# Optimization experiments

Hardware: AMD Instinct MI355X
Metric: run time of the kernel (lower is better)

## Reference

```python
import jax, jax.numpy as jnp
import numpy as np
import math

B, Hdim, Wdim, C = 8, 64, 64, 512
T, TXT = 77, 512
NH, HD = 8, 64  # num_heads, head_dim
TOP_M = 3
CLAMP_LOGIT = 2.0
CONF_THRESH = 0.35
NEG_INF = -1e30


def _ln(x, g, b, eps=1e-5):
    mu = x.mean(-1, keepdims=True)
    var = ((x - mu) ** 2).mean(-1, keepdims=True)
    return (x - mu) * jax.lax.rsqrt(var + eps) * g + b


def _l2norm(x, eps=1e-6):
    n = jnp.sqrt((x * x).sum(-1, keepdims=True))
    return x / jnp.maximum(n, eps)


def setup_inputs() -> dict:
    key = jax.random.key(0)
    ks = jax.random.split(key, 16)
    s = 0.02
    inp = {
        'visual_features': jax.random.normal(ks[0], (B, Hdim, Wdim, C), jnp.float32),
        'text_features': jax.random.normal(ks[1], (B, T, TXT), jnp.float32),
        'ln1_g': jnp.ones((C,), jnp.float32), 'ln1_b': jnp.zeros((C,), jnp.float32),
        'ln2_g': jnp.ones((C,), jnp.float32), 'ln2_b': jnp.zeros((C,), jnp.float32),
        'Wq': jax.random.normal(ks[2], (C, C), jnp.float32) * s, 'bq': jnp.zeros((C,), jnp.float32),
        'Wk': jax.random.normal(ks[3], (TXT, C), jnp.float32) * s, 'bk': jnp.zeros((C,), jnp.float32),
        'Wv': jax.random.normal(ks[4], (TXT, C), jnp.float32) * s, 'bv': jnp.zeros((C,), jnp.float32),
        'Wo': jax.random.normal(ks[5], (C, C), jnp.float32) * s, 'bo': jnp.zeros((C,), jnp.float32),
        'Wg': jax.random.normal(ks[6], (C, 1), jnp.float32) * s, 'bg': jnp.zeros((1,), jnp.float32),
        'W1': jax.random.normal(ks[7], (C, 4 * C), jnp.float32) * s, 'b1': jnp.zeros((4 * C,), jnp.float32),
        'W2': jax.random.normal(ks[8], (4 * C, C), jnp.float32) * s, 'b2': jnp.zeros((C,), jnp.float32),
        'logit_scale': jnp.asarray(math.log(1.0 / 0.07), jnp.float32),
        'alpha': jnp.asarray(0.1, jnp.float32),
    }
    return inp


def reference(visual_features, text_features, ln1_g, ln1_b, ln2_g, ln2_b,
              Wq, bq, Wk, bk, Wv, bv, Wo, bo, Wg, bg, W1, b1, W2, b2,
              logit_scale, alpha):
    b, h, w, c = visual_features.shape
    n = h * w
    # Pre-LN on visual tokens
    x = _ln(visual_features, ln1_g, ln1_b).reshape(b, n, c)
    q_full = x @ Wq + bq                                   # [B,N,C]
    pad_mask = jnp.abs(text_features).sum(-1) <= 1e-6      # [B,T]
    k_full = text_features @ Wk + bk                       # [B,T,C]
    v_full = text_features @ Wv + bv
    # l2-normalize over full channel dim, then split heads
    q = _l2norm(q_full).reshape(b, n, NH, HD)
    k = _l2norm(k_full).reshape(b, T, NH, HD)
    v = v_full.reshape(b, T, NH, HD)
    scale = jnp.exp(jnp.clip(logit_scale, -CLAMP_LOGIT, CLAMP_LOGIT)) / math.sqrt(float(HD))
    sim = jnp.einsum('bnhd,bthd->bnht', q, k) * scale      # [B,N,H,T]
    sim = jnp.where(pad_mask[:, None, None, :], NEG_INF, sim)
    # top-k sparsification: keep top_m per (b,n,h) row
    topv = jax.lax.top_k(sim, TOP_M)[0][..., -1:]
    sim = jnp.where(sim >= topv, sim, NEG_INF)
    attn = jax.nn.softmax(sim, axis=-1)
    attn = attn / jnp.maximum(attn.sum(-1, keepdims=True), 1e-6)
    all_pad = pad_mask.all(axis=1)                         # [B]
    attn = jnp.where(all_pad[:, None, None, None], 0.0, attn)
    # confidence: max-prob * (1 - normalized entropy), mean over heads
    attn_hn = attn.transpose(0, 2, 1, 3)                   # [B,H,N,T]
    maxp = attn_hn.max(-1, keepdims=True)
    t_eff = jnp.maximum((attn_hn > 0).astype(jnp.float32).sum(-1, keepdims=True), 2.0)
    p = jnp.maximum(attn_hn, 1e-8)
    entropy = jnp.maximum(-(p * jnp.log(p)).sum(-1, keepdims=True) / jnp.log(t_eff), 0.0)
    conf = jnp.clip(maxp * (1.0 - entropy), 0.0, 1.0).mean(axis=1)  # [B,N,1]
    bypass = (conf >= CONF_THRESH).astype(attn.dtype)
    aligned = jnp.einsum('bnht,bthd->bnhd', attn, v).reshape(b, n, c)
    aligned = (aligned @ Wo + bo) * bypass
    gate = jax.nn.sigmoid(x @ Wg + bg)                     # [B,N,1]
    y = x + alpha * gate * aligned
    y = _ln(y, ln2_g, ln2_b)
    y = y + (jax.nn.gelu(y @ W1 + b1, approximate=False) @ W2 + b2)
    return y.reshape(b, h, w, c)
```

## Files before the change

kernel.cpp:

```cpp
#include <hip/hip_runtime.h>
#include <stdint.h>

#define BATCH 8
#define NTOK 4096
#define CDIM 512
#define TTXT 77
#define TPAD 80
#define NHEAD 8
#define HDIM 64
#define HID 2048
#define MROWS 32768
#define NEGINF (-1e30f)

typedef __attribute__((ext_vector_type(8))) short short8;
typedef __attribute__((ext_vector_type(4))) float f32x4;

__device__ __forceinline__ float b2f(unsigned short u) {
    union { unsigned int i; float f; } x; x.i = ((unsigned int)u) << 16; return x.f;
}
__device__ __forceinline__ unsigned short f2b(float f) {
    union { float f; unsigned int i; } x; x.f = f;
    unsigned int i = x.i;
    return (unsigned short)((i + 0x7fffu + ((i >> 16) & 1u)) >> 16);
}

__device__ __forceinline__ void gload16(const void* g, void* l) {
    __builtin_amdgcn_global_load_lds(
        (const __attribute__((address_space(1))) unsigned int*)g,
        (__attribute__((address_space(3))) unsigned int*)l, 16, 0, 0);
}

#define OFF_WQT   ((size_t)0)
#define OFF_WKT   (OFF_WQT + 512*512*2)
#define OFF_WVT   (OFF_WKT + 512*512*2)
#define OFF_WOT   (OFF_WVT + 512*512*2)
#define OFF_W1T   (OFF_WOT + 512*512*2)
#define OFF_W2T   (OFF_W1T + (size_t)2048*512*2)
#define OFF_TEXTB (OFF_W2T + (size_t)512*2048*2)
#define OFF_KFB   (OFF_TEXTB + (size_t)640*512*2)
#define OFF_KNRM  (OFF_KFB + (size_t)640*512*2)
#define OFF_VPAD  (OFF_KNRM + (size_t)640*512*2)
#define OFF_PADM  (OFF_VPAD + (size_t)640*512*2)
#define OFF_ALLP  (OFF_PADM + 2560)
#define OFF_GATE  (OFF_ALLP + 256)
#define OFF_BYP   (OFF_GATE + (size_t)MROWS*4)
#define OFF_XB    (OFF_BYP + (size_t)MROWS*4)
#define OFF_BUFB  (OFF_XB + (size_t)MROWS*CDIM*2)
#define OFF_BUFC  (OFF_BUFB + (size_t)MROWS*CDIM*2)
#define OFF_H     (OFF_BUFC + (size_t)MROWS*CDIM*2)
#define WS_NEED   (OFF_H + (size_t)MROWS*HID*2)
#define OFF_VT    OFF_H

__device__ __forceinline__ float waveReduceAdd(float v) {
#pragma unroll
    for (int m = 1; m < 64; m <<= 1) v += __shfl_xor(v, m);
    return v;
}
__device__ __forceinline__ float waveReduceMin(float v) {
#pragma unroll
    for (int m = 1; m < 64; m <<= 1) v = fminf(v, __shfl_xor(v, m));
    return v;
}
__device__ __forceinline__ float red16Max(float v) {
#pragma unroll
    for (int m = 1; m < 16; m <<= 1) v = fmaxf(v, __shfl_xor(v, m));
    return v;
}
__device__ __forceinline__ float red16Add(float v) {
#pragma unroll
    for (int m = 1; m < 16; m <<= 1) v += __shfl_xor(v, m);
    return v;
}

__global__ __launch_bounds__(256) void transpose_kernel(
    const float* __restrict__ in, unsigned short* __restrict__ out, int R, int C)
{
    __shared__ float tile[32][33];
    const int tx = threadIdx.x & 31, ty = threadIdx.x >> 5;
    const int c0 = blockIdx.x * 32, r0 = blockIdx.y * 32;
#pragma unroll
    for (int i = 0; i < 32; i += 8)
        tile[ty + i][tx] = in[(size_t)(r0 + ty + i) * C + c0 + tx];
    __syncthreads();
#pragma unroll
    for (int i = 0; i < 32; i += 8)
        out[(size_t)(c0 + ty + i) * R + r0 + tx] = f2b(tile[tx][ty + i]);
}

__global__ __launch_bounds__(128) void text_prep_kernel(
    const float* __restrict__ text, unsigned short* __restrict__ textb, float* __restrict__ padm)
{
    __shared__ float sred[2];
    const int r = blockIdx.x;
    const int b = r / TPAD, t = r % TPAD;
    const int tid = threadIdx.x;
    if (t < TTXT) {
        float4 v = *(const float4*)(text + ((size_t)(b * TTXT + t)) * 512 + tid * 4);
        float a = fabsf(v.x) + fabsf(v.y) + fabsf(v.z) + fabsf(v.w);
        a = waveReduceAdd(a);
        if ((tid & 63) == 0) sred[tid >> 6] = a;
        __syncthreads();
        float asum = sred[0] + sred[1];
        ushort4 o; o.x = f2b(v.x); o.y = f2b(v.y); o.z = f2b(v.z); o.w = f2b(v.w);
        *(ushort4*)(textb + (size_t)r * 512 + tid * 4) = o;
        if (tid == 0) padm[r] = (asum <= 1e-6f) ? 1.f : 0.f;
    } else {
        ushort4 z; z.x = 0; z.y = 0; z.z = 0; z.w = 0;
        *(ushort4*)(textb + (size_t)r * 512 + tid * 4) = z;
        if (tid == 0) padm[r] = 1.f;
    }
}

__global__ __launch_bounds__(128) void allpad_kernel(
    const float* __restrict__ padm, float* __restrict__ allp)
{
    __shared__ float sred[2];
    const int b = blockIdx.x, tid = threadIdx.x;
    float f = (tid < TTXT) ? padm[b * TPAD + tid] : 1.f;
    f = waveReduceMin(f);
    if ((tid & 63) == 0) sred[tid >> 6] = f;
    __syncthreads();
    if (tid == 0) allp[b] = fminf(sred[0], sred[1]);
}

__global__ __launch_bounds__(128) void ln1_gate_kernel(
    const float* __restrict__ vin, const float* __restrict__ g1, const float* __restrict__ b1v,
    const float* __restrict__ Wg, const float* __restrict__ bg,
    unsigned short* __restrict__ xb, float* __restrict__ gate)
{
    __shared__ float sred[4];
    const int row = blockIdx.x, tid = threadIdx.x;
    const float4 v = *(const float4*)(vin + (size_t)row * 512 + tid * 4);
    float s = v.x + v.y + v.z + v.w;
    float s2 = v.x * v.x + v.y * v.y + v.z * v.z + v.w * v.w;
    s = waveReduceAdd(s); s2 = waveReduceAdd(s2);
    if ((tid & 63) == 0) { sred[tid >> 6] = s; sred[2 + (tid >> 6)] = s2; }
    __syncthreads();
    s = sred[0] + sred[1]; s2 = sred[2] + sred[3];
    const float mu = s * (1.f / 512.f);
    float var = s2 * (1.f / 512.f) - mu * mu;
    const float rs = rsqrtf(fmaxf(var, 0.f) + 1e-5f);
    const float4 gg = *(const float4*)(g1 + tid * 4);
    const float4 bb = *(const float4*)(b1v + tid * 4);
    const float x0 = (v.x - mu) * rs * gg.x + bb.x;
    const float x1 = (v.y - mu) * rs * gg.y + bb.y;
    const float x2 = (v.z - mu) * rs * gg.z + bb.z;
    const float x3 = (v.w - mu) * rs * gg.w + bb.w;
    ushort4 o; o.x = f2b(x0); o.y = f2b(x1); o.z = f2b(x2); o.w = f2b(x3);
    *(ushort4*)(xb + (size_t)row * 512 + tid * 4) = o;
    const float4 wg = *(const float4*)(Wg + tid * 4);
    float gp = x0 * wg.x + x1 * wg.y + x2 * wg.z + x3 * wg.w;
    gp = waveReduceAdd(gp);
    __syncthreads();
    if ((tid & 63) == 0) sred[tid >> 6] = gp;
    __syncthreads();
    if (tid == 0) {
        float z = sred[0] + sred[1] + bg[0];
        gate[row] = 1.f / (1.f + __expf(-z));
    }
}

__global__ __launch_bounds__(128) void ln2_kernel(
    const unsigned short* __restrict__ yin, const float* __restrict__ g2, const float* __restrict__ b2v,
    unsigned short* __restrict__ yb)
{
    __shared__ float sred[4];
    const int row = blockIdx.x, tid = threadIdx.x;
    ushort4 u = *(const ushort4*)(yin + (size_t)row * 512 + tid * 4);
    float v0 = b2f(u.x), v1 = b2f(u.y), v2 = b2f(u.z), v3 = b2f(u.w);
    float s = v0 + v1 + v2 + v3;
    float s2 = v0 * v0 + v1 * v1 + v2 * v2 + v3 * v3;
    s = waveReduceAdd(s); s2 = waveReduceAdd(s2);
    if ((tid & 63) == 0) { sred[tid >> 6] = s; sred[2 + (tid >> 6)] = s2; }
    __syncthreads();
    s = sred[0] + sred[1]; s2 = sred[2] + sred[3];
    const float mu = s * (1.f / 512.f);
    float var = s2 * (1.f / 512.f) - mu * mu;
    const float rs = rsqrtf(fmaxf(var, 0.f) + 1e-5f);
    const float4 gg = *(const float4*)(g2 + tid * 4);
    const float4 bb = *(const float4*)(b2v + tid * 4);
    ushort4 o;
    o.x = f2b((v0 - mu) * rs * gg.x + bb.x);
    o.y = f2b((v1 - mu) * rs * gg.y + bb.y);
    o.z = f2b((v2 - mu) * rs * gg.z + bb.z);
    o.w = f2b((v3 - mu) * rs * gg.w + bb.w);
    *(ushort4*)(yb + (size_t)row * 512 + tid * 4) = o;
}

__global__ __launch_bounds__(128) void l2norm_kernel(
    const unsigned short* __restrict__ in, unsigned short* __restrict__ out)
{
    __shared__ float sred[2];
    const int row = blockIdx.x, tid = threadIdx.x;
    ushort4 u = *(const ushort4*)(in + (size_t)row * 512 + tid * 4);
    float v0 = b2f(u.x), v1 = b2f(u.y), v2 = b2f(u.z), v3 = b2f(u.w);
    float ss = v0 * v0 + v1 * v1 + v2 * v2 + v3 * v3;
    ss = waveReduceAdd(ss);
    if ((tid & 63) == 0) sred[tid >> 6] = ss;
    __syncthreads();
    ss = sred[0] + sred[1];
    const float inv = 1.f / fmaxf(sqrtf(ss), 1e-6f);
    ushort4 o;
    o.x = f2b(v0 * inv); o.y = f2b(v1 * inv); o.z = f2b(v2 * inv); o.w = f2b(v3 * inv);
    *(ushort4*)(out + (size_t)row * 512 + tid * 4) = o;
}

__global__ __launch_bounds__(256) void vt_prep_kernel(
    const unsigned short* __restrict__ vp, unsigned short* __restrict__ vt)
{
    __shared__ unsigned short st[80][72];
    const int b = blockIdx.x >> 3, h = blockIdx.x & 7;
    const int tid = threadIdx.x;
    for (int idx = tid; idx < 80 * 64; idx += 256) {
        int t = idx >> 6, d = idx & 63;
        st[t][d] = vp[((size_t)(b * TPAD + t)) * 512 + h * 64 + d];
    }
    __syncthreads();
    for (int idx = tid; idx < 64 * 96; idx += 256) {
        int d = idx / 96, t = idx - d * 96;
        vt[((size_t)blockIdx.x * 64 + d) * 96 + t] = (t < TPAD) ? st[t][d] : (unsigned short)0;
    }
}

__global__ __launch_bounds__(256) void gemm_bt(
    const unsigned short* __restrict__ A, const unsigned short* __restrict__ Bt,
    const float* __restrict__ bias,
    unsigned short* __restrict__ outb, int M, int N, int K)
{
    __shared__ unsigned short sA[128 * 64];
    __shared__ unsigned short sB[128 * 64];
    char* cA = (char*)sA;
    char* cB = (char*)sB;
    const int tid = threadIdx.x;
    const int lane = tid & 63, w = tid >> 6;
    const int g = lane >> 4, ln = lane & 15;
    const int WR = w >> 1, WC = w & 1;
    const int rowA0 = blockIdx.x * 128, colB0 = blockIdx.y * 128;

    f32x4 acc[4][4];
#pragma unroll
    for (int m = 0; m < 4; ++m)
#pragma unroll
        for (int n = 0; n < 4; ++n) acc[m][n] = (f32x4){0.f, 0.f, 0.f, 0.f};

    for (int k0 = 0; k0 < K; k0 += 64) {
        __syncthreads();
#pragma unroll
        for (int i = 0; i < 4; ++i) {
            int c = tid + i * 256;
            int row = c >> 3, kc = c & 7;
            int kcs = kc ^ (row & 7);
            gload16(A + (size_t)(rowA0 + row) * K + k0 + kcs * 8, cA + c * 16);
            gload16(Bt + (size_t)(colB0 + row) * K + k0 + kcs * 8, cB + c * 16);
        }
        __syncthreads();
#pragma unroll
        for (int kk = 0; kk < 2; ++kk) {
            short8 af[4], bf[4];
#pragma unroll
            for (int m = 0; m < 4; ++m) {
                int row = WR * 64 + m * 16 + ln;
                af[m] = *(const short8*)(cA + row * 128 + ((kk * 64 + g * 16) ^ ((row & 7) << 4)));
            }
#pragma unroll
            for (int n = 0; n < 4; ++n) {
                int col = WC * 64 + n * 16 + ln;
                bf[n] = *(const short8*)(cB + col * 128 + ((kk * 64 + g * 16) ^ ((col & 7) << 4)));
            }
#pragma unroll
            for (int m = 0; m < 4; ++m)
#pragma unroll
                for (int n = 0; n < 4; ++n)
                    acc[m][n] = __builtin_amdgcn_mfma_f32_16x16x32_bf16(af[m], bf[n], acc[m][n], 0, 0, 0);
        }
    }

#pragma unroll
    for (int m = 0; m < 4; ++m) {
        const int rbase = rowA0 + WR * 64 + m * 16 + g * 4;
#pragma unroll
        for (int n = 0; n < 4; ++n) {
            const int col = colB0 + WC * 64 + n * 16 + ln;
            const float bcol = bias[col];
#pragma unroll
            for (int i = 0; i < 4; ++i)
                outb[(size_t)(rbase + i) * N + col] = f2b(acc[m][n][i] + bcol);
        }
    }
}

template<int EPI>
__global__ __launch_bounds__(512, 2) void gemm256(
    const unsigned short* __restrict__ A, const unsigned short* __restrict__ Bt,
    const float* __restrict__ bias,
    unsigned short* __restrict__ outb, float* __restrict__ outf,
    int M, int N, int K,
    const unsigned short* __restrict__ xres, const float* __restrict__ gate,
    const float* __restrict__ byp, const unsigned short* __restrict__ yres,
    const float* __restrict__ alphaPtr, int gxM, int gyN)
{
    __shared__ unsigned short lds[2][2][16384];
    const int tid = threadIdx.x;
    const int lane = tid & 63, w = tid >> 6;
    const int g = lane >> 4, ln = lane & 15;
    const int wr = w >> 2, wc = w & 3;

    int bm, bn;
    {
        const int L = (int)blockIdx.x;
        const int xcd = L & 7, j = L >> 3;
        const int rl = j / gyN;
        bn = j - rl * gyN;
        bm = xcd * (gxM >> 3) + rl;
    }
    const int rowA0 = bm * 256, colB0 = bn * 256;
    const int nt = K >> 6;

    auto stageA = [&](int t, int mh) {
        const int buf = t & 1;
#pragma unroll
        for (int r = 0; r < 2; ++r) {
            const int c = tid + r * 512;
            const int prl = c >> 3, kc = c & 7;
            const int grow = rowA0 + ((prl >> 6) << 7) + (mh << 6) + (prl & 63);
            gload16(A + (size_t)grow * K + (t << 6) + ((kc ^ (prl & 7)) << 3),
                    (char*)&lds[buf][0][mh * 8192] + c * 16);
        }
    };
    auto stageB = [&](int t, int nh) {
        const int buf = t & 1;
#pragma unroll
        for (int r = 0; r < 2; ++r) {
            const int c = tid + r * 512;
            const int prl = c >> 3, kc = c & 7;
            const int gcol = colB0 + ((prl >> 5) << 6) + (nh << 5) + (prl & 31);
            gload16(Bt + (size_t)gcol * K + (t << 6) + ((kc ^ (prl & 7)) << 3),
                    (char*)&lds[buf][1][nh * 8192] + c * 16);
        }
    };

    f32x4 acc[8][4];
#pragma unroll
    for (int m = 0; m < 8; ++m)
#pragma unroll
        for (int n = 0; n < 4; ++n) acc[m][n] = (f32x4){0.f, 0.f, 0.f, 0.f};

    stageA(0, 0); stageB(0, 0); stageB(0, 1); stageA(0, 1);
    stageA(1, 0); stageB(1, 0); stageB(1, 1);
    asm volatile("s_waitcnt vmcnt(6)" ::: "memory");
    __builtin_amdgcn_s_barrier();

    const int sw  = (ln & 7) << 4;
    const int kb0 = (g * 16) ^ sw;
    const int kb1 = (64 + g * 16) ^ sw;
    const int arow = (wr * 64 + ln) * 128;
    const int brow = (wc * 32 + ln) * 128;

    short8 afr[4][2], bfr[4][2];

    for (int t = 0; t < nt; ++t) {
        const char* lA = (const char*)&lds[t & 1][0][0];
        const char* lB = (const char*)&lds[t & 1][1][0];

#pragma unroll
        for (int m = 0; m < 4; ++m) {
            afr[m][0] = *(const short8*)(lA + arow + m * 2048 + kb0);
            afr[m][1] = *(const short8*)(lA + arow + m * 2048 + kb1);
        }
#pragma unroll
        for (int n = 0; n < 2; ++n) {
            bfr[n][0] = *(const short8*)(lB + brow + n * 2048 + kb0);
            bfr[n][1] = *(const short8*)(lB + brow + n * 2048 + kb1);
        }
        if (t + 1 < nt) stageA(t + 1, 1);
        __builtin_amdgcn_s_barrier();
        __builtin_amdgcn_s_setprio(1);
#pragma unroll
        for (int m = 0; m < 4; ++m)
#pragma unroll
            for (int n = 0; n < 2; ++n) {
                acc[m][n] = __builtin_amdgcn_mfma_f32_16x16x32_bf16(afr[m][0], bfr[n][0], acc[m][n], 0, 0, 0);
                acc[m][n] = __builtin_amdgcn_mfma_f32_16x16x32_bf16(afr[m][1], bfr[n][1], acc[m][n], 0, 0, 0);
            }
        __builtin_amdgcn_s_setprio(0);
        __builtin_amdgcn_s_barrier();

#pragma unroll
        for (int n = 2; n < 4; ++n) {
            bfr[n][0] = *(const short8*)(lB + brow + (n & 1) * 2048 + 16384 + kb0);
            bfr[n][1] = *(const short8*)(lB + brow + (n & 1) * 2048 + 16384 + kb1);
        }
        if (t + 2 < nt) stageA(t + 2, 0);
        __builtin_amdgcn_s_barrier();
        __builtin_amdgcn_s_setprio(1);
#pragma unroll
        for (int m = 0; m < 4; ++m)
#pragma unroll
            for (int n = 2; n < 4; ++n) {
                acc[m][n] = __builtin_amdgcn_mfma_f32_16x16x32_bf16(afr[m][0], bfr[n][0], acc[m][n], 0, 0, 0);
                acc[m][n] = __builtin_amdgcn_mfma_f32_16x16x32_bf16(afr[m][1], bfr[n][1], acc[m][n], 0, 0, 0);
            }
        __builtin_amdgcn_s_setprio(0);
        __builtin_amdgcn_s_barrier();

#pragma unroll
        for (int m = 0; m < 4; ++m) {
            afr[m][0] = *(const short8*)(lA + arow + m * 2048 + 16384 + kb0);
            afr[m][1] = *(const short8*)(lA + arow + m * 2048 + 16384 + kb1);
        }
        if (t + 2 < nt) stageB(t + 2, 0);
        __builtin_amdgcn_s_barrier();
        __builtin_amdgcn_s_setprio(1);
#pragma unroll
        for (int m = 0; m < 4; ++m)
#pragma unroll
            for (int n = 0; n < 2; ++n) {
                acc[m + 4][n] = __builtin_amdgcn_mfma_f32_16x16x32_bf16(afr[m][0], bfr[n][0], acc[m + 4][n], 0, 0, 0);
                acc[m + 4][n] = __builtin_amdgcn_mfma_f32_16x16x32_bf16(afr[m][1], bfr[n][1], acc[m + 4][n], 0, 0, 0);
            }
        __builtin_amdgcn_s_setprio(0);
        __builtin_amdgcn_s_barrier();

        if (t + 2 < nt) stageB(t + 2, 1);
        if (t == nt - 2) { asm volatile("s_waitcnt vmcnt(0)" ::: "memory"); }
        else             { asm volatile("s_waitcnt vmcnt(6)" ::: "memory"); }
        __builtin_amdgcn_s_barrier();
        __builtin_amdgcn_s_setprio(1);
#pragma unroll
        for (int m = 0; m < 4; ++m)
#pragma unroll
            for (int n = 2; n < 4; ++n) {
                acc[m + 4][n] = __builtin_amdgcn_mfma_f32_16x16x32_bf16(afr[m][0], bfr[n][0], acc[m + 4][n], 0, 0, 0);
                acc[m + 4][n] = __builtin_amdgcn_mfma_f32_16x16x32_bf16(afr[m][1], bfr[n][1], acc[m + 4][n], 0, 0, 0);
            }
        __builtin_amdgcn_s_setprio(0);
        __builtin_amdgcn_s_barrier();
    }

    const float alpha = (EPI == 1) ? *alphaPtr : 0.f;
#pragma unroll
    for (int m = 0; m < 8; ++m) {
        const int rbase = rowA0 + wr * 128 + m * 16 + g * 4;
#pragma unroll
        for (int n = 0; n < 4; ++n) {
            const int col = colB0 + wc * 64 + n * 16 + ln;
            const float bcol = bias[col];
#pragma unroll
            for (int i = 0; i < 4; ++i) {
                const int row = rbase + i;
                const float v = acc[m][n][i] + bcol;
                if (EPI == 0) {
                    outb[(size_t)row * N + col] = f2b(v);
                } else if (EPI == 1) {
                    float yp = b2f(xres[(size_t)row * N + col]) + alpha * gate[row] * byp[row] * v;
                    outb[(size_t)row * N + col] = f2b(yp);
                } else if (EPI == 2) {
                    const float u2 = 2.f * v * (0.7978845608f + 0.0356774081f * v * v);
                    const float tt = 1.f - 2.f / (__expf(u2) + 1.f);
                    outb[(size_t)row * N + col] = f2b(0.5f * v * (1.f + tt));
                } else {
                    outf[(size_t)row * N + col] = b2f(yres[(size_t)row * N + col]) + v;
                }
            }
        }
    }
}

__global__ __launch_bounds__(256) void attn_kernel(
    const unsigned short* __restrict__ qn,
    const unsigned short* __restrict__ kn,
    const unsigned short* __restrict__ vt,
    const float* __restrict__ padm,
    const float* __restrict__ allp,
    const float* __restrict__ lscPtr,
    unsigned short* __restrict__ aligned,
    float* __restrict__ bypass)
{
    const int b = blockIdx.y;
    const int n0 = blockIdx.x * 16;
    const int tid = threadIdx.x;
    const int w = tid >> 6, lane = tid & 63, g = lane >> 4, ln = lane & 15;
    __shared__ unsigned short s_p[4][16][104];
    __shared__ float s_conf[4][16];

    if (allp[b] > 0.5f) {
        uint4 z = {0u, 0u, 0u, 0u};
#pragma unroll
        for (int j = 0; j < 4; ++j) {
            int id = tid + j * 256;
            int row = id >> 6, c8 = id & 63;
            *(uint4*)(aligned + ((size_t)(b * NTOK + n0 + row)) * 512 + c8 * 8) = z;
        }
        if (tid < 16) bypass[b * NTOK + n0 + tid] = 0.f;
        return;
    }

    float lscale;
    {
        float ls = *lscPtr;
        ls = fminf(fmaxf(ls, -2.f), 2.f);
        lscale = __expf(ls) * 0.125f;
    }

    float pm[5];
#pragma unroll
    for (int tt = 0; tt < 5; ++tt) {
        int t = ln + tt * 16;
        pm[tt] = (t < TTXT) ? padm[b * TPAD + t] : 1.f;
    }

    for (int j = g; j < 24; j += 4) s_p[w][ln][80 + j] = 0;

    float conf_acc[4] = {0.f, 0.f, 0.f, 0.f};
    const size_t qrow = ((size_t)(b * NTOK + n0 + ln)) * 512;

#pragma unroll
    for (int hh = 0; hh < 2; ++hh) {
        const int h = w + hh * 4;
        short8 a0 = *(const short8*)(qn + qrow + h * 64 + g * 8);
        short8 a1 = *(const short8*)(qn + qrow + h * 64 + 32 + g * 8);
        f32x4 sim[5];
#pragma unroll
        for (int tt = 0; tt < 5; ++tt) {
            const size_t kbase = ((size_t)(b * TPAD + tt * 16 + ln)) * 512 + h * 64;
            short8 b0 = *(const short8*)(kn + kbase + g * 8);
            short8 b1 = *(const short8*)(kn + kbase + 32 + g * 8);
            f32x4 c = (f32x4){0.f, 0.f, 0.f, 0.f};
            c = __builtin_amdgcn_mfma_f32_16x16x32_bf16(a0, b0, c, 0, 0, 0);
            c = __builtin_amdgcn_mfma_f32_16x16x32_bf16(a1, b1, c, 0, 0, 0);
            sim[tt] = c;
        }
#pragma unroll
        for (int i = 0; i < 4; ++i) {
            float v[5];
#pragma unroll
            for (int tt = 0; tt < 5; ++tt)
                v[tt] = (pm[tt] == 0.f) ? sim[tt][i] * lscale : NEGINF;

            float lm = v[0];
#pragma unroll
            for (int tt = 1; tt < 5; ++tt) lm = fmaxf(lm, v[tt]);
            const float m1 = red16Max(lm);
            float lm2 = -3.0e38f;
#pragma unroll
            for (int tt = 0; tt < 5; ++tt) if (v[tt] < m1) lm2 = fmaxf(lm2, v[tt]);
            const float m2 = red16Max(lm2);
            float lm3 = -3.0e38f;
#pragma unroll
            for (int tt = 0; tt < 5; ++tt) if (v[tt] < m2) lm3 = fmaxf(lm3, v[tt]);
            const float m3 = red16Max(lm3);
            float lc1 = 0.f, lc2 = 0.f;
#pragma unroll
            for (int tt = 0; tt < 5; ++tt) {
                if (v[tt] >= m1) lc1 += 1.f;
                if (v[tt] >= m2) lc2 += 1.f;
            }
            const float c1 = red16Add(lc1);
            const float c2 = red16Add(lc2);
            const float th = (c1 >= 3.f) ? m1 : ((c2 >= 3.f) ? m2 : m3);

            float p[5], lsum = 0.f, lcnt = 0.f;
#pragma unroll
            for (int tt = 0; tt < 5; ++tt) {
                float pv = (v[tt] >= th) ? __expf(v[tt] - m1) : 0.f;
                p[tt] = pv;
                lsum += pv;
                lcnt += (pv > 0.f) ? 1.f : 0.f;
            }
            const float psum = red16Add(lsum);
            const float pcnt = red16Add(lcnt);
            const float inv = 1.f / fmaxf(psum, 1e-20f);

            float lmaxp = 0.f, lent = 0.f;
#pragma unroll
            for (int tt = 0; tt < 5; ++tt) {
                float a = p[tt] * inv;
                p[tt] = a;
                lmaxp = fmaxf(lmaxp, a);
                if (a > 0.f) {
                    float pp = fmaxf(a, 1e-8f);
                    lent += -pp * __logf(pp);
                }
            }
            const float maxp = red16Max(lmaxp);
            float ent = red16Add(lent);
            ent += (77.f - pcnt) * 1.8420680744e-7f;
            const float teff = fmaxf(pcnt, 2.f);
            const float entropy = fmaxf(ent / __logf(teff), 0.f);
            const float confh = fminf(fmaxf(maxp * (1.f - entropy), 0.f), 1.f);
            conf_acc[i] += confh;

#pragma unroll
            for (int tt = 0; tt < 5; ++tt)
                s_p[w][g * 4 + i][ln + tt * 16] = f2b(p[tt]);
        }
        short8 af[3];
#pragma unroll
        for (int k = 0; k < 3; ++k)
            af[k] = *(const short8*)(&s_p[w][ln][k * 32 + g * 8]);
        const size_t vtb = ((size_t)(b * NHEAD + h)) * 64;
#pragma unroll
        for (int n = 0; n < 4; ++n) {
            f32x4 o = (f32x4){0.f, 0.f, 0.f, 0.f};
#pragma unroll
            for (int k = 0; k < 3; ++k) {
                short8 bf = *(const short8*)(vt + (vtb + n * 16 + ln) * 96 + k * 32 + g * 8);
                o = __builtin_amdgcn_mfma_f32_16x16x32_bf16(af[k], bf, o, 0, 0, 0);
            }
#pragma unroll
            for (int i = 0; i < 4; ++i)
                aligned[((size_t)(b * NTOK + n0 + g * 4 + i)) * 512 + h * 64 + n * 16 + ln] =
                    f2b(o[i]);
        }
    }

    if (ln == 0) {
#pragma unroll
        for (int i = 0; i < 4; ++i) s_conf[w][g * 4 + i] = conf_acc[i];
    }
    __syncthreads();
    if (tid < 16) {
        float c = (s_conf[0][tid] + s_conf[1][tid] + s_conf[2][tid] + s_conf[3][tid]) * 0.125f;
        bypass[b * NTOK + n0 + tid] = (c >= 0.35f) ? 1.f : 0.f;
    }
}

extern "C" void kernel_launch(void* const* d_in, const int* in_sizes, int n_in,
                              void* d_out, int out_size, void* d_ws, size_t ws_size,
                              hipStream_t stream)
{
    (void)in_sizes; (void)n_in; (void)out_size;
    if (ws_size < WS_NEED) return;

    const float* visual = (const float*)d_in[0];
    const float* text   = (const float*)d_in[1];
    const float* ln1_g  = (const float*)d_in[2];
    const float* ln1_b  = (const float*)d_in[3];
    const float* ln2_g  = (const float*)d_in[4];
    const float* ln2_b  = (const float*)d_in[5];
    const float* Wq = (const float*)d_in[6];   const float* bq = (const float*)d_in[7];
    const float* Wk = (const float*)d_in[8];   const float* bk = (const float*)d_in[9];
    const float* Wv = (const float*)d_in[10];  const float* bv = (const float*)d_in[11];
    const float* Wo = (const float*)d_in[12];  const float* bo = (const float*)d_in[13];
    const float* Wg = (const float*)d_in[14];  const float* bg = (const float*)d_in[15];
    const float* W1 = (const float*)d_in[16];  const float* b1 = (const float*)d_in[17];
    const float* W2 = (const float*)d_in[18];  const float* b2 = (const float*)d_in[19];
    const float* lsc = (const float*)d_in[20];
    const float* alp = (const float*)d_in[21];

    char* ws = (char*)d_ws;
    unsigned short* WQT  = (unsigned short*)(ws + OFF_WQT);
    unsigned short* WKT  = (unsigned short*)(ws + OFF_WKT);
    unsigned short* WVT  = (unsigned short*)(ws + OFF_WVT);
    unsigned short* WOT  = (unsigned short*)(ws + OFF_WOT);
    unsigned short* W1T  = (unsigned short*)(ws + OFF_W1T);
    unsigned short* W2T  = (unsigned short*)(ws + OFF_W2T);
    unsigned short* TEXTB = (unsigned short*)(ws + OFF_TEXTB);
    unsigned short* KFB  = (unsigned short*)(ws + OFF_KFB);
    unsigned short* KNRM = (unsigned short*)(ws + OFF_KNRM);
    unsigned short* VPAD = (unsigned short*)(ws + OFF_VPAD);
    float* PADM = (float*)(ws + OFF_PADM);
    float* ALLP = (float*)(ws + OFF_ALLP);
    float* GATE = (float*)(ws + OFF_GATE);
    float* BYP  = (float*)(ws + OFF_BYP);
    unsigned short* XB   = (unsigned short*)(ws + OFF_XB);
    unsigned short* BUFB = (unsigned short*)(ws + OFF_BUFB);
    unsigned short* BUFC = (unsigned short*)(ws + OFF_BUFC);
    unsigned short* HBUF = (unsigned short*)(ws + OFF_H);
    unsigned short* VT   = (unsigned short*)(ws + OFF_VT);
    float* out = (float*)d_out;

    transpose_kernel<<<dim3(16, 16), 256, 0, stream>>>(Wq, WQT, 512, 512);
    transpose_kernel<<<dim3(16, 16), 256, 0, stream>>>(Wk, WKT, 512, 512);
    transpose_kernel<<<dim3(16, 16), 256, 0, stream>>>(Wv, WVT, 512, 512);
    transpose_kernel<<<dim3(16, 16), 256, 0, stream>>>(Wo, WOT, 512, 512);
    transpose_kernel<<<dim3(64, 16), 256, 0, stream>>>(W1, W1T, 512, 2048);
    transpose_kernel<<<dim3(16, 64), 256, 0, stream>>>(W2, W2T, 2048, 512);

    text_prep_kernel<<<640, 128, 0, stream>>>(text, TEXTB, PADM);
    allpad_kernel<<<BATCH, 128, 0, stream>>>(PADM, ALLP);

    ln1_gate_kernel<<<MROWS, 128, 0, stream>>>(visual, ln1_g, ln1_b, Wg, bg, XB, GATE);

    gemm_bt<<<dim3(5, 4), 256, 0, stream>>>(TEXTB, WKT, bk, KFB, 640, 512, 512);
    gemm_bt<<<dim3(5, 4), 256, 0, stream>>>(TEXTB, WVT, bv, VPAD, 640, 512, 512);
    l2norm_kernel<<<640, 128, 0, stream>>>(KFB, KNRM);
    vt_prep_kernel<<<BATCH * NHEAD, 256, 0, stream>>>(VPAD, VT);

    gemm256<0><<<dim3(128 * 2), 512, 0, stream>>>(XB, WQT, bq, BUFB, nullptr, MROWS, 512, 512,
                                                  nullptr, nullptr, nullptr, nullptr, nullptr,
                                                  128, 2);
    l2norm_kernel<<<MROWS, 128, 0, stream>>>(BUFB, BUFC);

    attn_kernel<<<dim3(NTOK / 16, BATCH), 256, 0, stream>>>(BUFC, KNRM, VT, PADM, ALLP, lsc,
                                                            BUFB, BYP);

    gemm256<1><<<dim3(128 * 2), 512, 0, stream>>>(BUFB, WOT, bo, BUFC, nullptr, MROWS, 512, 512,
                                                  XB, GATE, BYP, nullptr, alp, 128, 2);

    ln2_kernel<<<MROWS, 128, 0, stream>>>(BUFC, ln2_g, ln2_b, XB);

    gemm256<2><<<dim3(128 * 8), 512, 0, stream>>>(XB, W1T, b1, HBUF, nullptr, MROWS, HID, 512,
                                                  nullptr, nullptr, nullptr, nullptr, nullptr,
                                                  128, 8);
    gemm256<3><<<dim3(128 * 2), 512, 0, stream>>>(HBUF, W2T, b2, nullptr, out, MROWS, 512, HID,
                                                  nullptr, nullptr, nullptr, XB, nullptr,
                                                  128, 2);
}
```

Before: 398.5 us.

## Merge weight transposes, simplify GEMM staging, and stage epilogue through LDS

Six weight-transpose launches are merged into one kernel that picks its source matrix from the block index, cutting launch overhead. The 256x256 GEMM precomputes its global and LDS staging addresses, splits fragment loads into two k-halves around the barrier, and unrolls the k-loop by two to cut address arithmetic and overlap LDS reads with MFMA. The epilogue now writes accumulators to LDS (unioned with the tile buffers) and reads them back row-major, so bias loads, residual reads and output stores are vectorized and coalesced instead of strided scalar accesses. The extra barriers and LDS round trip per 16-row slab add synchronization cost in exchange.

```diff
diff --git a/kernel.cpp b/kernel.cpp
--- a/kernel.cpp
+++ b/kernel.cpp
@@ -72,19 +72,34 @@
     return v;
 }
 
-__global__ __launch_bounds__(256) void transpose_kernel(
-    const float* __restrict__ in, unsigned short* __restrict__ out, int R, int C)
+__global__ __launch_bounds__(256) void transpose_all_kernel(
+    const float* __restrict__ Wq, const float* __restrict__ Wk,
+    const float* __restrict__ Wv, const float* __restrict__ Wo,
+    const float* __restrict__ W1, const float* __restrict__ W2,
+    unsigned short* __restrict__ WQT, unsigned short* __restrict__ WKT,
+    unsigned short* __restrict__ WVT, unsigned short* __restrict__ WOT,
+    unsigned short* __restrict__ W1T, unsigned short* __restrict__ W2T)
 {
     __shared__ float tile[32][33];
+    int b = blockIdx.x;
+    const float* src; unsigned short* dst; int R, C, cx, ry;
+    if (b < 1024)       { src = W1; dst = W1T; R = 512;  C = 2048; cx = b & 63; ry = b >> 6; }
+    else if (b < 2048)  { b -= 1024; src = W2; dst = W2T; R = 2048; C = 512; cx = b & 15; ry = b >> 4; }
+    else {
+        b -= 2048; const int which = b >> 8; b &= 255;
+        R = 512; C = 512; cx = b & 15; ry = b >> 4;
+        src = (which == 0) ? Wq : (which == 1) ? Wk : (which == 2) ? Wv : Wo;
+        dst = (which == 0) ? WQT : (which == 1) ? WKT : (which == 2) ? WVT : WOT;
+    }
     const int tx = threadIdx.x & 31, ty = threadIdx.x >> 5;
-    const int c0 = blockIdx.x * 32, r0 = blockIdx.y * 32;
+    const int c0 = cx * 32, r0 = ry * 32;
 #pragma unroll
     for (int i = 0; i < 32; i += 8)
-        tile[ty + i][tx] = in[(size_t)(r0 + ty + i) * C + c0 + tx];
+        tile[ty + i][tx] = src[(size_t)(r0 + ty + i) * C + c0 + tx];
     __syncthreads();
 #pragma unroll
     for (int i = 0; i < 32; i += 8)
-        out[(size_t)(c0 + ty + i) * R + r0 + tx] = f2b(tile[tx][ty + i]);
+        dst[(size_t)(c0 + ty + i) * R + r0 + tx] = f2b(tile[tx][ty + i]);
 }
 
 __global__ __launch_bounds__(128) void text_prep_kernel(
@@ -289,6 +304,19 @@
     }
 }
 
+#define STAGE_A(tt, mh) do {                                                        \
+    gload16(aBase + (mh) * K64 + (size_t)(tt) * 64,                                 \
+            &lds.t[(tt) & 1][0][(mh) * 1024 + tid]);                                \
+    gload16(aBase + (2 + (mh)) * K64 + (size_t)(tt) * 64,                           \
+            &lds.t[(tt) & 1][0][(mh) * 1024 + tid + 512]);                          \
+} while (0)
+#define STAGE_B(tt, nh) do {                                                        \
+    gload16(bBase + (nh) * K32 + (size_t)(tt) * 64,                                 \
+            &lds.t[(tt) & 1][1][(nh) * 1024 + tid]);                                \
+    gload16(bBase + (4 + (nh)) * K32 + (size_t)(tt) * 64,                           \
+            &lds.t[(tt) & 1][1][(nh) * 1024 + tid + 512]);                          \
+} while (0)
+
 template<int EPI>
 __global__ __launch_bounds__(512, 2) void gemm256(
     const unsigned short* __restrict__ A, const unsigned short* __restrict__ Bt,
@@ -299,7 +327,10 @@
     const float* __restrict__ byp, const unsigned short* __restrict__ yres,
     const float* __restrict__ alphaPtr, int gxM, int gyN)
 {
-    __shared__ unsigned short lds[2][2][16384];
+    __shared__ union ULds {
+        uint4 t[2][2][2048];
+        float e[32 * 260];
+    } lds;
     const int tid = threadIdx.x;
     const int lane = tid & 63, w = tid >> 6;
     const int g = lane >> 4, ln = lane & 15;
@@ -316,28 +347,17 @@
     const int rowA0 = bm * 256, colB0 = bn * 256;
     const int nt = K >> 6;
 
-    auto stageA = [&](int t, int mh) {
-        const int buf = t & 1;
-#pragma unroll
-        for (int r = 0; r < 2; ++r) {
-            const int c = tid + r * 512;
-            const int prl = c >> 3, kc = c & 7;
-            const int grow = rowA0 + ((prl >> 6) << 7) + (mh << 6) + (prl & 63);
-            gload16(A + (size_t)grow * K + (t << 6) + ((kc ^ (prl & 7)) << 3),
-                    (char*)&lds[buf][0][mh * 8192] + c * 16);
-        }
-    };
-    auto stageB = [&](int t, int nh) {
-        const int buf = t & 1;
-#pragma unroll
-        for (int r = 0; r < 2; ++r) {
-            const int c = tid + r * 512;
-            const int prl = c >> 3, kc = c & 7;
-            const int gcol = colB0 + ((prl >> 5) << 6) + (nh << 5) + (prl & 31);
-            gload16(Bt + (size_t)gcol * K + (t << 6) + ((kc ^ (prl & 7)) << 3),
-                    (char*)&lds[buf][1][nh * 8192] + c * 16);
-        }
-    };
+    const int p0 = tid >> 3;
+    const int swzk = (tid & 7) ^ (p0 & 7);
+    const size_t sK = (size_t)K;
+    const size_t K64 = sK * 64, K32 = sK * 32;
+    const unsigned short* aBase = A + (size_t)(rowA0 + p0) * sK + swzk * 8;
+    const unsigned short* bBase = Bt + (size_t)(colB0 + ((p0 >> 5) << 6) + (p0 & 31)) * sK + swzk * 8;
+
+    const int kb0 = g ^ (ln & 7);
+    const int kb1 = (4 + g) ^ (ln & 7);
+    const int ar = (wr * 64 + ln) * 8;
+    const int br = (wc * 32 + ln) * 8;
 
     f32x4 acc[8][4];
 #pragma unroll
@@ -345,83 +365,81 @@
 #pragma unroll
         for (int n = 0; n < 4; ++n) acc[m][n] = (f32x4){0.f, 0.f, 0.f, 0.f};
 
-    stageA(0, 0); stageB(0, 0); stageB(0, 1); stageA(0, 1);
-    stageA(1, 0); stageB(1, 0); stageB(1, 1);
+    STAGE_A(0, 0); STAGE_B(0, 0); STAGE_B(0, 1); STAGE_A(0, 1);
+    STAGE_A(1, 0); STAGE_B(1, 0); STAGE_B(1, 1);
     asm volatile("s_waitcnt vmcnt(6)" ::: "memory");
     __builtin_amdgcn_s_barrier();
 
-    const int sw  = (ln & 7) << 4;
-    const int kb0 = (g * 16) ^ sw;
-    const int kb1 = (64 + g * 16) ^ sw;
-    const int arow = (wr * 64 + ln) * 128;
-    const int brow = (wc * 32 + ln) * 128;
-
-    short8 afr[4][2], bfr[4][2];
-
+    short8 a0[4], a1[4], b0[4], b1[4];
+
+#pragma unroll 2
     for (int t = 0; t < nt; ++t) {
-        const char* lA = (const char*)&lds[t & 1][0][0];
-        const char* lB = (const char*)&lds[t & 1][1][0];
-
-#pragma unroll
-        for (int m = 0; m < 4; ++m) {
-            afr[m][0] = *(const short8*)(lA + arow + m * 2048 + kb0);
-            afr[m][1] = *(const short8*)(lA + arow + m * 2048 + kb1);
-        }
-#pragma unroll
-        for (int n = 0; n < 2; ++n) {
-            bfr[n][0] = *(const short8*)(lB + brow + n * 2048 + kb0);
-            bfr[n][1] = *(const short8*)(lB + brow + n * 2048 + kb1);
-        }
-        if (t + 1 < nt) stageA(t + 1, 1);
-        __builtin_amdgcn_s_barrier();
+        const int buf = t & 1;
+#pragma unroll
+        for (int m = 0; m < 4; ++m) a0[m] = *(const short8*)&lds.t[buf][0][ar + m * 128 + kb0];
+        b0[0] = *(const short8*)&lds.t[buf][1][br + kb0];
+        b0[1] = *(const short8*)&lds.t[buf][1][br + 128 + kb0];
+        if (t + 1 < nt) STAGE_A(t + 1, 1);
+        __builtin_amdgcn_s_barrier();
+#pragma unroll
+        for (int m = 0; m < 4; ++m) a1[m] = *(const short8*)&lds.t[buf][0][ar + m * 128 + kb1];
+        b1[0] = *(const short8*)&lds.t[buf][1][br + kb1];
+        b1[1] = *(const short8*)&lds.t[buf][1][br + 128 + kb1];
         __builtin_amdgcn_s_setprio(1);
 #pragma unroll
         for (int m = 0; m < 4; ++m)
 #pragma unroll
-            for (int n = 0; n < 2; ++n) {
-                acc[m][n] = __builtin_amdgcn_mfma_f32_16x16x32_bf16(afr[m][0], bfr[n][0], acc[m][n], 0, 0, 0);
-                acc[m][n] = __builtin_amdgcn_mfma_f32_16x16x32_bf16(afr[m][1], bfr[n][1], acc[m][n], 0, 0, 0);
-            }
+            for (int n = 0; n < 2; ++n)
+                acc[m][n] = __builtin_amdgcn_mfma_f32_16x16x32_bf16(a0[m], b0[n], acc[m][n], 0, 0, 0);
+#pragma unroll
+        for (int m = 0; m < 4; ++m)
+#pragma unroll
+            for (int n = 0; n < 2; ++n)
+                acc[m][n] = __builtin_amdgcn_mfma_f32_16x16x32_bf16(a1[m], b1[n], acc[m][n], 0, 0, 0);
         __builtin_amdgcn_s_setprio(0);
         __builtin_amdgcn_s_barrier();
 
-#pragma unroll
-        for (int n = 2; n < 4; ++n) {
-            bfr[n][0] = *(const short8*)(lB + brow + (n & 1) * 2048 + 16384 + kb0);
-            bfr[n][1] = *(const short8*)(lB + brow + (n & 1) * 2048 + 16384 + kb1);
-        }
-        if (t + 2 < nt) stageA(t + 2, 0);
-        __builtin_amdgcn_s_barrier();
+        b0[2] = *(const short8*)&lds.t[buf][1][1024 + br + kb0];
+        b0[3] = *(const short8*)&lds.t[buf][1][1024 + br + 128 + kb0];
+        if (t + 2 < nt) STAGE_A(t + 2, 0);
+        __builtin_amdgcn_s_barrier();
+        b1[2] = *(const short8*)&lds.t[buf][1][1024 + br + kb1];
+        b1[3] = *(const short8*)&lds.t[buf][1][1024 + br + 128 + kb1];
         __builtin_amdgcn_s_setprio(1);
 #pragma unroll
         for (int m = 0; m < 4; ++m)
 #pragma unroll
-            for (int n = 2; n < 4; ++n) {
-                acc[m][n] = __builtin_amdgcn_mfma_f32_16x16x32_bf16(afr[m][0], bfr[n][0], acc[m][n], 0, 0, 0);
-                acc[m][n] = __builtin_amdgcn_mfma_f32_16x16x32_bf16(afr[m][1], bfr[n][1], acc[m][n], 0, 0, 0);
-            }
+            for (int n = 2; n < 4; ++n)
+                acc[m][n] = __builtin_amdgcn_mfma_f32_16x16x32_bf16(a0[m], b0[n], acc[m][n], 0, 0, 0);
+#pragma unroll
+        for (int m = 0; m < 4; ++m)
+#pragma unroll
+            for (int n = 2; n < 4; ++n)
+                acc[m][n] = __builtin_amdgcn_mfma_f32_16x16x32_bf16(a1[m], b1[n], acc[m][n], 0, 0, 0);
         __builtin_amdgcn_s_setprio(0);
         __builtin_amdgcn_s_barrier();
 
 #pragma unroll
-        for (int m = 0; m < 4; ++m) {
-            afr[m][0] = *(const short8*)(lA + arow + m * 2048 + 16384 + kb0);
-            afr[m][1] = *(const short8*)(lA + arow + m * 2048 + 16384 + kb1);
-        }
-        if (t + 2 < nt) stageB(t + 2, 0);
-        __builtin_amdgcn_s_barrier();
+        for (int m = 0; m < 4; ++m) a0[m] = *(const short8*)&lds.t[buf][0][1024 + ar + m * 128 + kb0];
+        if (t + 2 < nt) STAGE_B(t + 2, 0);
+        __builtin_amdgcn_s_barrier();
+#pragma unroll
+        for (int m = 0; m < 4; ++m) a1[m] = *(const short8*)&lds.t[buf][0][1024 + ar + m * 128 + kb1];
         __builtin_amdgcn_s_setprio(1);
 #pragma unroll
         for (int m = 0; m < 4; ++m)
 #pragma unroll
-            for (int n = 0; n < 2; ++n) {
-                acc[m + 4][n] = __builtin_amdgcn_mfma_f32_16x16x32_bf16(afr[m][0], bfr[n][0], acc[m + 4][n], 0, 0, 0);
-                acc[m + 4][n] = __builtin_amdgcn_mfma_f32_16x16x32_bf16(afr[m][1], bfr[n][1], acc[m + 4][n], 0, 0, 0);
-            }
+            for (int n = 0; n < 2; ++n)
+                acc[m + 4][n] = __builtin_amdgcn_mfma_f32_16x16x32_bf16(a0[m], b0[n], acc[m + 4][n], 0, 0, 0);
+#pragma unroll
+        for (int m = 0; m < 4; ++m)
+#pragma unroll
+            for (int n = 0; n < 2; ++n)
+                acc[m + 4][n] = __builtin_amdgcn_mfma_f32_16x16x32_bf16(a1[m], b1[n], acc[m + 4][n], 0, 0, 0);
         __builtin_amdgcn_s_setprio(0);
         __builtin_amdgcn_s_barrier();
 
-        if (t + 2 < nt) stageB(t + 2, 1);
+        if (t + 2 < nt) STAGE_B(t + 2, 1);
         if (t == nt - 2) { asm volatile("s_waitcnt vmcnt(0)" ::: "memory"); }
         else             { asm volatile("s_waitcnt vmcnt(6)" ::: "memory"); }
         __builtin_amdgcn_s_barrier();
@@ -429,42 +447,78 @@
 #pragma unroll
         for (int m = 0; m < 4; ++m)
 #pragma unroll
-            for (int n = 2; n < 4; ++n) {
-                acc[m + 4][n] = __builtin_amdgcn_mfma_f32_16x16x32_bf16(afr[m][0], bfr[n][0], acc[m + 4][n], 0, 0, 0);
-                acc[m + 4][n] = __builtin_amdgcn_mfma_f32_16x16x32_bf16(afr[m][1], bfr[n][1], acc[m + 4][n], 0, 0, 0);
-            }
+            for (int n = 2; n < 4; ++n)
+                acc[m + 4][n] = __builtin_amdgcn_mfma_f32_16x16x32_bf16(a0[m], b0[n], acc[m + 4][n], 0, 0, 0);
+#pragma unroll
+        for (int m = 0; m < 4; ++m)
+#pragma unroll
+            for (int n = 2; n < 4; ++n)
+                acc[m + 4][n] = __builtin_amdgcn_mfma_f32_16x16x32_bf16(a1[m], b1[n], acc[m + 4][n], 0, 0, 0);
         __builtin_amdgcn_s_setprio(0);
         __builtin_amdgcn_s_barrier();
     }
 
     const float alpha = (EPI == 1) ? *alphaPtr : 0.f;
+    const int er = tid >> 4;
+    const int ec = (tid & 15) * 4;
+    const int grow0 = rowA0 + (er >> 4) * 128 + (er & 15);
 #pragma unroll
     for (int m = 0; m < 8; ++m) {
-        const int rbase = rowA0 + wr * 128 + m * 16 + g * 4;
-#pragma unroll
-        for (int n = 0; n < 4; ++n) {
-            const int col = colB0 + wc * 64 + n * 16 + ln;
-            const float bcol = bias[col];
-#pragma unroll
-            for (int i = 0; i < 4; ++i) {
-                const int row = rbase + i;
-                const float v = acc[m][n][i] + bcol;
-                if (EPI == 0) {
-                    outb[(size_t)row * N + col] = f2b(v);
-                } else if (EPI == 1) {
-                    float yp = b2f(xres[(size_t)row * N + col]) + alpha * gate[row] * byp[row] * v;
-                    outb[(size_t)row * N + col] = f2b(yp);
-                } else if (EPI == 2) {
-                    const float u2 = 2.f * v * (0.7978845608f + 0.0356774081f * v * v);
+        __builtin_amdgcn_s_barrier();
+#pragma unroll
+        for (int n = 0; n < 4; ++n)
+#pragma unroll
+            for (int i = 0; i < 4; ++i)
+                lds.e[(wr * 16 + g * 4 + i) * 260 + wc * 64 + n * 16 + ln] = acc[m][n][i];
+        __builtin_amdgcn_s_barrier();
+        const int grow = grow0 + m * 16;
+        float gb = 0.f;
+        if (EPI == 1) gb = alpha * gate[grow] * byp[grow];
+#pragma unroll
+        for (int rep = 0; rep < 4; ++rep) {
+            const int lcol = rep * 64 + ec;
+            const int col = colB0 + lcol;
+            f32x4 v = *(const f32x4*)&lds.e[er * 260 + lcol];
+            const f32x4 bc = *(const f32x4*)&bias[col];
+            v = v + bc;
+            const size_t oidx = (size_t)grow * N + col;
+            if (EPI == 0) {
+                ushort4 o;
+                o.x = f2b(v[0]); o.y = f2b(v[1]); o.z = f2b(v[2]); o.w = f2b(v[3]);
+                *(ushort4*)&outb[oidx] = o;
+            } else if (EPI == 1) {
+                const ushort4 xr = *(const ushort4*)&xres[oidx];
+                ushort4 o;
+                o.x = f2b(b2f(xr.x) + gb * v[0]);
+                o.y = f2b(b2f(xr.y) + gb * v[1]);
+                o.z = f2b(b2f(xr.z) + gb * v[2]);
+                o.w = f2b(b2f(xr.w) + gb * v[3]);
+                *(ushort4*)&outb[oidx] = o;
+            } else if (EPI == 2) {
+                ushort4 o;
+#pragma unroll
+                for (int j = 0; j < 4; ++j) {
+                    const float x = v[j];
+                    const float u2 = 2.f * x * (0.7978845608f + 0.0356774081f * x * x);
                     const float tt = 1.f - 2.f / (__expf(u2) + 1.f);
-                    outb[(size_t)row * N + col] = f2b(0.5f * v * (1.f + tt));
-                } else {
-                    outf[(size_t)row * N + col] = b2f(yres[(size_t)row * N + col]) + v;
+                    const float h = 0.5f * x * (1.f + tt);
+                    ((unsigned short*)&o)[j] = f2b(h);
                 }
+                *(ushort4*)&outb[oidx] = o;
+            } else {
+                const ushort4 yr = *(const ushort4*)&yres[oidx];
+                f32x4 of;
+                of[0] = b2f(yr.x) + v[0];
+                of[1] = b2f(yr.y) + v[1];
+                of[2] = b2f(yr.z) + v[2];
+                of[3] = b2f(yr.w) + v[3];
+                *(f32x4*)&outf[oidx] = of;
             }
         }
     }
 }
+#undef STAGE_A
+#undef STAGE_B
 
 __global__ __launch_bounds__(256) void attn_kernel(
     const unsigned short* __restrict__ qn,
@@ -670,12 +724,8 @@
     unsigned short* VT   = (unsigned short*)(ws + OFF_VT);
     float* out = (float*)d_out;
 
-    transpose_kernel<<<dim3(16, 16), 256, 0, stream>>>(Wq, WQT, 512, 512);
-    transpose_kernel<<<dim3(16, 16), 256, 0, stream>>>(Wk, WKT, 512, 512);
-    transpose_kernel<<<dim3(16, 16), 256, 0, stream>>>(Wv, WVT, 512, 512);
-    transpose_kernel<<<dim3(16, 16), 256, 0, stream>>>(Wo, WOT, 512, 512);
-    transpose_kernel<<<dim3(64, 16), 256, 0, stream>>>(W1, W1T, 512, 2048);
-    transpose_kernel<<<dim3(16, 64), 256, 0, stream>>>(W2, W2T, 2048, 512);
+    transpose_all_kernel<<<3072, 256, 0, stream>>>(Wq, Wk, Wv, Wo, W1, W2,
+                                                   WQT, WKT, WVT, WOT, W1T, W2T);
 
     text_prep_kernel<<<640, 128, 0, stream>>>(text, TEXTB, PADM);
     allpad_kernel<<<BATCH, 128, 0, stream>>>(PADM, ALLP);
```

Result: no change. 400.0 us (+0.4%).
